# Performance work log

Hardware: AMD Instinct MI355X
Metric: run time of the kernel (lower is better)

## Reference

```python
import jax, jax.numpy as jnp
import numpy as np

B, C_IN, N, K = 4, 128, 2048, 16
DIM, POS, PH, AH = 256, 3, 64, 256 * 4
EPS = 1e-5


def _conv1x1(x, W, b):
    # 1x1 Conv2d: x (B, Cin, n, k) -> (B, Cout, n, k)
    return jnp.einsum('oc,bcnk->bonk', W, x) + b[None, :, None, None]


def _bn(x, gamma, beta, mean, var):
    # eval-mode BatchNorm2d with running stats
    scale = gamma / jnp.sqrt(var + EPS)
    return x * scale[None, :, None, None] + (beta - mean * scale)[None, :, None, None]


def _forward(key, values, pos, Wk, bk, Wq, bq, Wv, bv,
             Wp1, bp1, pg, pb, pm, pv, Wp2, bp2,
             Wa1, ba1, ag, ab, am, av, Wa2, ba2, We, be):
    b, _, n, k = key.shape
    pos_f = jnp.broadcast_to(pos[:, :, :, None], (b, pos.shape[1], n, k))
    kf = _conv1x1(key, Wk, bk)          # (B, dim, n, k)
    v = _conv1x1(values, Wv, bv)        # (B, dim, n, k)
    q = _conv1x1(pos_f, Wq, bq)         # (B, dim, n, k)
    qk_rel = q - kf
    pe = _conv1x1(jax.nn.relu(_bn(_conv1x1(q, Wp1, bp1), pg, pb, pm, pv)), Wp2, bp2)
    attn = _conv1x1(jax.nn.relu(_bn(_conv1x1(qk_rel * pe + pe, Wa1, ba1), ag, ab, am, av)), Wa2, ba2)
    attn = jax.nn.softmax(attn, axis=-1)  # softmax over k neighbors
    agg = jnp.einsum('bcnk,bcnk->bcn', attn, v + pe)  # (B, dim, n)
    return jnp.einsum('oc,bcn->bon', We, agg) + be[None, :, None]


def setup_inputs():
    ks = jax.random.split(jax.random.key(0), 12)
    s = 0.02
    f32 = jnp.float32
    return {
        'key': jax.random.normal(ks[0], (B, C_IN, N, K), f32),
        'values': jax.random.normal(ks[1], (B, C_IN, N, K), f32),
        'pos': jax.random.normal(ks[2], (B, POS, N), f32),
        'Wk': jax.random.normal(ks[3], (DIM, C_IN), f32) * s,
        'bk': jnp.zeros((DIM,), f32),
        'Wq': jax.random.normal(ks[4], (DIM, POS), f32) * s,
        'bq': jnp.zeros((DIM,), f32),
        'Wv': jax.random.normal(ks[5], (DIM, C_IN), f32) * s,
        'bv': jnp.zeros((DIM,), f32),
        'Wp1': jax.random.normal(ks[6], (PH, DIM), f32) * s,
        'bp1': jnp.zeros((PH,), f32),
        'pg': jnp.ones((PH,), f32),
        'pb': jnp.zeros((PH,), f32),
        'pm': jnp.zeros((PH,), f32),
        'pv': jnp.ones((PH,), f32),
        'Wp2': jax.random.normal(ks[7], (DIM, PH), f32) * s,
        'bp2': jnp.zeros((DIM,), f32),
        'Wa1': jax.random.normal(ks[8], (AH, DIM), f32) * s,
        'ba1': jnp.zeros((AH,), f32),
        'ag': jnp.ones((AH,), f32),
        'ab': jnp.zeros((AH,), f32),
        'am': jnp.zeros((AH,), f32),
        'av': jnp.ones((AH,), f32),
        'Wa2': jax.random.normal(ks[9], (DIM, AH), f32) * s,
        'ba2': jnp.zeros((DIM,), f32),
        'We': jax.random.normal(ks[10], (DIM, DIM), f32) * s,
        'be': jnp.zeros((DIM,), f32),
    }


def reference(key, values, pos, Wk, bk, Wq, bq, Wv, bv,
              Wp1, bp1, pg, pb, pm, pv, Wp2, bp2,
              Wa1, ba1, ag, ab, am, av, Wa2, ba2, We, be):
    return _forward(key, values, pos, Wk, bk, Wq, bq, Wv, bv,
                    Wp1, bp1, pg, pb, pm, pv, Wp2, bp2,
                    Wa1, ba1, ag, ab, am, av, Wa2, ba2, We, be)
```

## Files before the change

kernel.cpp:

```cpp
#include <hip/hip_runtime.h>
#include <math.h>

typedef __attribute__((ext_vector_type(8))) short bf16x8;
typedef __attribute__((ext_vector_type(4))) float f32x4;

namespace {
constexpr int NN   = 2048;
constexpr float EPSV = 1e-5f;

constexpr size_t WK_O   = 0;
constexpr size_t WV_O   = 65536;
constexpr size_t B1F_O  = 131072;
constexpr size_t WEP_O  = 135168;
constexpr size_t WA1I_O = 266240;
constexpr size_t WA2I_O = 790528;
constexpr size_t WP1Q_O = 1314816;
constexpr size_t SC_O   = 1315840;
constexpr size_t WS_TOTAL = 1319936;

constexpr int X_OFF   = 0;
constexpr int WC_OFF  = 65536;
constexpr int WA2C_OFF= 98304;
constexpr int HR_OFF  = 131072;
constexpr int PE_OFF  = 147456;
constexpr int H1_OFF  = 151552;
constexpr int POS_OFF = 153600;
constexpr int LDS_TOTAL = 153728;
}

__device__ __forceinline__ unsigned short f2bf(float x) {
    unsigned u = __float_as_uint(x);
    unsigned r = (u + 0x7FFFu + ((u >> 16) & 1u)) >> 16;
    return (unsigned short)r;
}
__device__ __forceinline__ float bf2f(unsigned short h) {
    return __uint_as_float(((unsigned)h) << 16);
}


__global__ void prep_sc(const float* __restrict__ ag,  const float* __restrict__ ab,
                        const float* __restrict__ am,  const float* __restrict__ av,
                        const float* __restrict__ ba1,
                        const float* __restrict__ Wp1, const float* __restrict__ Wq,
                        const float* __restrict__ bq,  const float* __restrict__ bp1,
                        const float* __restrict__ pg,  const float* __restrict__ pb,
                        const float* __restrict__ pm,  const float* __restrict__ pv,
                        char* __restrict__ ws)
{
    const int t = threadIdx.x, blk = blockIdx.x;
    float* b1f  = (float*)(ws + B1F_O);
    float* sc_s = (float*)(ws + SC_O);
    float* wp1q = (float*)(ws + WP1Q_O);
    if (blk < 4) {
        int j = blk * 256 + t;
        float sc = ag[j] * rsqrtf(av[j] + EPSV);
        sc_s[j] = sc;
        b1f[j] = ba1[j] * sc + ab[j] - am[j] * sc;
    } else if (t < 64) {
        int ph = t;
        float scp = pg[ph] * rsqrtf(pv[ph] + EPSV);
        float a0 = 0.f, a1 = 0.f, a2 = 0.f, abv = 0.f;
        for (int c = 0; c < 256; ++c) {
            float wv = Wp1[ph * 256 + c];
            a0 = fmaf(wv, Wq[c * 3 + 0], a0);
            a1 = fmaf(wv, Wq[c * 3 + 1], a1);
            a2 = fmaf(wv, Wq[c * 3 + 2], a2);
            abv = fmaf(wv, bq[c], abv);
        }
        wp1q[ph * 4 + 0] = scp * a0;
        wp1q[ph * 4 + 1] = scp * a1;
        wp1q[ph * 4 + 2] = scp * a2;
        wp1q[ph * 4 + 3] = scp * (abv + bp1[ph]) + (pb[ph] - pm[ph] * scp);
    }
}

__global__ void prep_cvt(const float* __restrict__ Wk, const float* __restrict__ Wv,
                         const float* __restrict__ We, const float* __restrict__ Wa1,
                         const float* __restrict__ Wa2, char* __restrict__ ws)
{
    const int idx = blockIdx.x * 256 + threadIdx.x;
    unsigned short* wk  = (unsigned short*)(ws + WK_O);
    unsigned short* wv  = (unsigned short*)(ws + WV_O);
    unsigned short* wep = (unsigned short*)(ws + WEP_O);
    unsigned short* w1i = (unsigned short*)(ws + WA1I_O);
    unsigned short* w2i = (unsigned short*)(ws + WA2I_O);
    const float* sc_s = (const float*)(ws + SC_O);
    if (idx < 32768) {
        wk[idx] = f2bf(Wk[idx]);
    } else if (idx < 65536) {
        int i = idx - 32768; wv[i] = f2bf(Wv[i]);
    } else if (idx < 131072) {
        int i = idx - 65536; wep[i] = f2bf(We[i]);
    } else if (idx < 393216) {
        int e = idx - 131072;
        int j = e >> 8, c = e & 255;
        float val = sc_s[j] * Wa1[e];
        int cc = j >> 6, jl = j & 63;
        int byte = cc * 32768 + (((jl << 9) + (c << 1)) ^ ((jl & 7) << 4));
        w1i[byte >> 1] = f2bf(val);
    } else {
        int e = idx - 393216;
        int o = e >> 10, j = e & 1023;
        int cc = j >> 6, jl = j & 63;
        int byte = cc * 32768 + (((o << 7) + (jl << 1)) ^ ((o & 7) << 4));
        w2i[byte >> 1] = f2bf(Wa2[e]);
    }
}

__global__ __launch_bounds__(256, 1)
void pt_main(const float* __restrict__ key, const float* __restrict__ values,
             const float* __restrict__ pos,
             const float* __restrict__ Wq,  const float* __restrict__ bq,
             const float* __restrict__ bk,  const float* __restrict__ bv,
             const float* __restrict__ Wp2, const float* __restrict__ bp2,
             const float* __restrict__ be,
             const char* __restrict__ ws,
             float* __restrict__ outp)
{
    extern __shared__ char sm[];
    const int t = threadIdx.x;
    const int w = t >> 6, l = t & 63;
    const int l15 = l & 15, lg = l >> 4;
    const int blk = blockIdx.x;
    const int b = blk >> 8;
    const int n0 = (blk & 255) * 8;
    const int wm0 = w * 32;

    const unsigned short* wkp = (const unsigned short*)(ws + WK_O);
    const unsigned short* wvp = (const unsigned short*)(ws + WV_O);
    const unsigned short* wep = (const unsigned short*)(ws + WEP_O);
    const float* b1f  = (const float*)(ws + B1F_O);
    const float* wp1q = (const float*)(ws + WP1Q_O);

    if (t < 24) {
        int nl = t / 3, p = t % 3;
        *(float*)(sm + POS_OFF + nl * 16 + p * 4) = pos[(b * 3 + p) * NN + n0 + nl];
    }
    {
        #pragma unroll
        for (int it = 0; it < 16; ++it) {
            int i = it * 256 + t;
            int clow = i & 7, k4 = (i >> 3) & 3, nl = (i >> 5) & 7, chigh = i >> 8;
            int c = chigh * 8 + clow;
            const float4 v = *(const float4*)(key + ((size_t)(b * 128 + c) * NN + (n0 + nl)) * 16 + k4 * 4);
            int m = nl * 16 + k4 * 4;
            #pragma unroll
            for (int j = 0; j < 4; ++j) {
                int mm = m + j;
                int byte = ((mm << 8) + (c << 1)) ^ ((mm & 7) << 4);
                float fj = (j == 0) ? v.x : (j == 1) ? v.y : (j == 2) ? v.z : v.w;
                *(unsigned short*)(sm + X_OFF + byte) = f2bf(fj);
            }
        }
    }
    __syncthreads();

    #pragma unroll
    for (int rep = 0; rep < 2; ++rep) {
        int idx = rep * 256 + t;
        int ph = idx >> 3, nl = idx & 7;
        const float4 wq4 = *(const float4*)(wp1q + ph * 4);
        float p0 = *(const float*)(sm + POS_OFF + nl * 16 + 0);
        float p1 = *(const float*)(sm + POS_OFF + nl * 16 + 4);
        float p2 = *(const float*)(sm + POS_OFF + nl * 16 + 8);
        float h = fmaf(wq4.x, p0, fmaf(wq4.y, p1, fmaf(wq4.z, p2, wq4.w)));
        *(float*)(sm + H1_OFF + ph * 32 + nl * 4) = fmaxf(h, 0.f);
    }
    __syncthreads();

    {
        float acc[8];
        #pragma unroll
        for (int n = 0; n < 8; ++n) acc[n] = 0.f;
        #pragma unroll 4
        for (int j = 0; j < 64; ++j) {
            float wv2 = Wp2[t * 64 + j];
            float4 ha = *(const float4*)(sm + H1_OFF + j * 32);
            float4 hb = *(const float4*)(sm + H1_OFF + j * 32 + 16);
            acc[0] = fmaf(wv2, ha.x, acc[0]); acc[1] = fmaf(wv2, ha.y, acc[1]);
            acc[2] = fmaf(wv2, ha.z, acc[2]); acc[3] = fmaf(wv2, ha.w, acc[3]);
            acc[4] = fmaf(wv2, hb.x, acc[4]); acc[5] = fmaf(wv2, hb.y, acc[5]);
            acc[6] = fmaf(wv2, hb.z, acc[6]); acc[7] = fmaf(wv2, hb.w, acc[7]);
        }
        float bp = bp2[t];
        #pragma unroll
        for (int n = 0; n < 8; ++n)
            *(unsigned short*)(sm + PE_OFF + n * 512 + t * 2) = f2bf(acc[n] + bp);
    }

    bf16x8 ak[2][4];
    #pragma unroll
    for (int mt = 0; mt < 2; ++mt)
        #pragma unroll
        for (int kt = 0; kt < 4; ++kt) {
            int m = wm0 + mt * 16 + l15, c = kt * 32 + lg * 8;
            ak[mt][kt] = *(const bf16x8*)(sm + X_OFF + (((m << 8) + (c << 1)) ^ ((m & 7) << 4)));
        }
    f32x4 zf = {0.f, 0.f, 0.f, 0.f};
    f32x4 kacc[2][16];
    #pragma unroll
    for (int mt = 0; mt < 2; ++mt)
        #pragma unroll
        for (int ot = 0; ot < 16; ++ot) kacc[mt][ot] = zf;
    #pragma unroll
    for (int ot = 0; ot < 16; ++ot) {
        #pragma unroll
        for (int kt = 0; kt < 4; ++kt) {
            int o = ot * 16 + l15, c = kt * 32 + lg * 8;
            bf16x8 bfr = *(const bf16x8*)(wkp + o * 128 + c);
            kacc[0][ot] = __builtin_amdgcn_mfma_f32_16x16x32_bf16(ak[0][kt], bfr, kacc[0][ot], 0, 0, 0);
            kacc[1][ot] = __builtin_amdgcn_mfma_f32_16x16x32_bf16(ak[1][kt], bfr, kacc[1][ot], 0, 0, 0);
        }
    }
    __syncthreads();

    #pragma unroll
    for (int mt = 0; mt < 2; ++mt) {
        const int nl = 2 * w + mt;
        float p0 = *(const float*)(sm + POS_OFF + nl * 16 + 0);
        float p1 = *(const float*)(sm + POS_OFF + nl * 16 + 4);
        float p2 = *(const float*)(sm + POS_OFF + nl * 16 + 8);
        #pragma unroll
        for (int ot = 0; ot < 16; ++ot) {
            int o = ot * 16 + l15;
            float q = fmaf(Wq[o * 3 + 0], p0, fmaf(Wq[o * 3 + 1], p1, fmaf(Wq[o * 3 + 2], p2, bq[o])));
            float pe = bf2f(*(const unsigned short*)(sm + PE_OFF + nl * 512 + o * 2));
            float bko = bk[o];
            #pragma unroll
            for (int r = 0; r < 4; ++r) {
                int m = wm0 + mt * 16 + lg * 4 + r;
                float x = (q - (kacc[mt][ot][r] + bko) + 1.f) * pe;
                *(unsigned short*)(sm + X_OFF + (((m << 9) + (o << 1)) ^ ((m & 7) << 4))) = f2bf(x);
            }
        }
    }

    f32x4 Y[2][16];
    #pragma unroll
    for (int mt = 0; mt < 2; ++mt)
        #pragma unroll
        for (int ot = 0; ot < 16; ++ot) Y[mt][ot] = zf;

    for (int cc = 0; cc < 16; ++cc) {
        if (cc) __syncthreads();
        {
            const float4* s1 = (const float4*)(ws + WA1I_O + (size_t)cc * 32768);
            float4* d1 = (float4*)(sm + WC_OFF);
            const float4* s2 = (const float4*)(ws + WA2I_O + (size_t)cc * 32768);
            float4* d2 = (float4*)(sm + WA2C_OFF);
            #pragma unroll
            for (int i = 0; i < 8; ++i) d1[i * 256 + t] = s1[i * 256 + t];
            #pragma unroll
            for (int i = 0; i < 8; ++i) d2[i * 256 + t] = s2[i * 256 + t];
        }
        __syncthreads();

        #pragma unroll
        for (int mt = 0; mt < 2; ++mt) {
            bf16x8 ax[8];
            #pragma unroll
            for (int kt = 0; kt < 8; ++kt) {
                int m = wm0 + mt * 16 + l15, c = kt * 32 + lg * 8;
                ax[kt] = *(const bf16x8*)(sm + X_OFF + (((m << 9) + (c << 1)) ^ ((m & 7) << 4)));
            }
            #pragma unroll
            for (int jt = 0; jt < 4; ++jt) {
                f32x4 acc = zf;
                #pragma unroll
                for (int kt = 0; kt < 8; ++kt) {
                    int jl = jt * 16 + l15, c2 = kt * 32 + lg * 8;
                    bf16x8 bw = *(const bf16x8*)(sm + WC_OFF + (((jl << 9) + (c2 << 1)) ^ ((jl & 7) << 4)));
                    acc = __builtin_amdgcn_mfma_f32_16x16x32_bf16(ax[kt], bw, acc, 0, 0, 0);
                }
                float b1v = b1f[cc * 64 + jt * 16 + l15];
                #pragma unroll
                for (int r = 0; r < 4; ++r) {
                    int ml = mt * 16 + lg * 4 + r, jl = jt * 16 + l15;
                    float hv = fmaxf(acc[r] + b1v, 0.f);
                    *(unsigned short*)(sm + HR_OFF + w * 4096 + (((ml << 7) + (jl << 1)) ^ ((ml & 7) << 4))) = f2bf(hv);
                }
            }
        }
        #pragma unroll
        for (int mt = 0; mt < 2; ++mt) {
            bf16x8 ah[2];
            #pragma unroll
            for (int kt = 0; kt < 2; ++kt) {
                int ml = mt * 16 + l15, jl = kt * 32 + lg * 8;
                ah[kt] = *(const bf16x8*)(sm + HR_OFF + w * 4096 + (((ml << 7) + (jl << 1)) ^ ((ml & 7) << 4)));
            }
            #pragma unroll
            for (int ot = 0; ot < 16; ++ot) {
                #pragma unroll
                for (int kt = 0; kt < 2; ++kt) {
                    int o = ot * 16 + l15, jl = kt * 32 + lg * 8;
                    bf16x8 bw = *(const bf16x8*)(sm + WA2C_OFF + (((o << 7) + (jl << 1)) ^ ((o & 7) << 4)));
                    Y[mt][ot] = __builtin_amdgcn_mfma_f32_16x16x32_bf16(ah[kt], bw, Y[mt][ot], 0, 0, 0);
                }
            }
        }
    }
    __syncthreads();

    {
        #pragma unroll
        for (int it = 0; it < 16; ++it) {
            int i = it * 256 + t;
            int clow = i & 7, k4 = (i >> 3) & 3, nl = (i >> 5) & 7, chigh = i >> 8;
            int c = chigh * 8 + clow;
            const float4 v = *(const float4*)(values + ((size_t)(b * 128 + c) * NN + (n0 + nl)) * 16 + k4 * 4);
            int m = nl * 16 + k4 * 4;
            #pragma unroll
            for (int j = 0; j < 4; ++j) {
                int mm = m + j;
                int byte = ((mm << 8) + (c << 1)) ^ ((mm & 7) << 4);
                float fj = (j == 0) ? v.x : (j == 1) ? v.y : (j == 2) ? v.z : v.w;
                *(unsigned short*)(sm + WC_OFF + byte) = f2bf(fj);
            }
        }
    }

    #pragma unroll
    for (int mt = 0; mt < 2; ++mt) {
        #pragma unroll
        for (int ot = 0; ot < 16; ++ot) {
            float mx = fmaxf(fmaxf(Y[mt][ot][0], Y[mt][ot][1]), fmaxf(Y[mt][ot][2], Y[mt][ot][3]));
            mx = fmaxf(mx, __shfl_xor(mx, 16));
            mx = fmaxf(mx, __shfl_xor(mx, 32));
            float e0 = expf(Y[mt][ot][0] - mx), e1 = expf(Y[mt][ot][1] - mx);
            float e2 = expf(Y[mt][ot][2] - mx), e3 = expf(Y[mt][ot][3] - mx);
            float s = e0 + e1 + e2 + e3;
            s += __shfl_xor(s, 16);
            s += __shfl_xor(s, 32);
            float inv = 1.f / s;
            Y[mt][ot][0] = e0 * inv; Y[mt][ot][1] = e1 * inv;
            Y[mt][ot][2] = e2 * inv; Y[mt][ot][3] = e3 * inv;
        }
    }
    __syncthreads();

    bf16x8 av_[2][4];
    #pragma unroll
    for (int mt = 0; mt < 2; ++mt)
        #pragma unroll
        for (int kt = 0; kt < 4; ++kt) {
            int m = wm0 + mt * 16 + l15, c = kt * 32 + lg * 8;
            av_[mt][kt] = *(const bf16x8*)(sm + WC_OFF + (((m << 8) + (c << 1)) ^ ((m & 7) << 4)));
        }
    #pragma unroll
    for (int ot = 0; ot < 16; ++ot) {
        int o = ot * 16 + l15;
        f32x4 vacc[2];
        vacc[0] = zf; vacc[1] = zf;
        #pragma unroll
        for (int kt = 0; kt < 4; ++kt) {
            int c = kt * 32 + lg * 8;
            bf16x8 bfr = *(const bf16x8*)(wvp + o * 128 + c);
            vacc[0] = __builtin_amdgcn_mfma_f32_16x16x32_bf16(av_[0][kt], bfr, vacc[0], 0, 0, 0);
            vacc[1] = __builtin_amdgcn_mfma_f32_16x16x32_bf16(av_[1][kt], bfr, vacc[1], 0, 0, 0);
        }
        float bvo = bv[o];
        #pragma unroll
        for (int mt = 0; mt < 2; ++mt) {
            int nl = 2 * w + mt;
            float s = 0.f;
            #pragma unroll
            for (int r = 0; r < 4; ++r)
                s = fmaf(Y[mt][ot][r], vacc[mt][r] + bvo, s);
            s += __shfl_xor(s, 16);
            s += __shfl_xor(s, 32);
            float agg = s + bf2f(*(const unsigned short*)(sm + PE_OFF + nl * 512 + o * 2));
            if (lg == 0)
                *(unsigned short*)(sm + X_OFF + (((nl << 9) + (o << 1)) ^ ((nl & 7) << 4))) = f2bf(agg);
        }
    }
    __syncthreads();

    bf16x8 aa[8];
    #pragma unroll
    for (int kt = 0; kt < 8; ++kt) {
        int row = l15, c = kt * 32 + lg * 8;
        aa[kt] = *(const bf16x8*)(sm + X_OFF + (((row << 9) + (c << 1)) ^ ((row & 7) << 4)));
    }
    #pragma unroll
    for (int ot = 0; ot < 4; ++ot) {
        int oo = w * 64 + ot * 16 + l15;
        f32x4 acc = zf;
        #pragma unroll
        for (int kt = 0; kt < 8; ++kt) {
            int c = kt * 32 + lg * 8;
            bf16x8 bfr = *(const bf16x8*)(wep + oo * 256 + c);
            acc = __builtin_amdgcn_mfma_f32_16x16x32_bf16(aa[kt], bfr, acc, 0, 0, 0);
        }
        if (lg < 2) {
            float bev = be[oo];
            float4 vv;
            vv.x = acc[0] + bev; vv.y = acc[1] + bev;
            vv.z = acc[2] + bev; vv.w = acc[3] + bev;
            *(float4*)(outp + ((size_t)(b * 256 + oo)) * NN + n0 + lg * 4) = vv;
        }
    }
}

extern "C" void kernel_launch(void* const* d_in, const int* in_sizes, int n_in,
                              void* d_out, int out_size, void* d_ws, size_t ws_size,
                              hipStream_t stream) {
    const float* key    = (const float*)d_in[0];
    const float* values = (const float*)d_in[1];
    const float* pos    = (const float*)d_in[2];
    const float* Wk     = (const float*)d_in[3];
    const float* bk     = (const float*)d_in[4];
    const float* Wq     = (const float*)d_in[5];
    const float* bq     = (const float*)d_in[6];
    const float* Wv     = (const float*)d_in[7];
    const float* bv     = (const float*)d_in[8];
    const float* Wp1    = (const float*)d_in[9];
    const float* bp1    = (const float*)d_in[10];
    const float* pg     = (const float*)d_in[11];
    const float* pb     = (const float*)d_in[12];
    const float* pm     = (const float*)d_in[13];
    const float* pv     = (const float*)d_in[14];
    const float* Wp2    = (const float*)d_in[15];
    const float* bp2    = (const float*)d_in[16];
    const float* Wa1    = (const float*)d_in[17];
    const float* ba1    = (const float*)d_in[18];
    const float* ag     = (const float*)d_in[19];
    const float* ab     = (const float*)d_in[20];
    const float* am     = (const float*)d_in[21];
    const float* av     = (const float*)d_in[22];
    const float* Wa2    = (const float*)d_in[23];
    const float* We     = (const float*)d_in[25];
    const float* be     = (const float*)d_in[26];
    (void)in_sizes; (void)n_in; (void)out_size; (void)ws_size;

    char* ws = (char*)d_ws;

    hipFuncSetAttribute((const void*)pt_main,
                        hipFuncAttributeMaxDynamicSharedMemorySize, LDS_TOTAL);

    hipLaunchKernelGGL(prep_sc, dim3(5), dim3(256), 0, stream,
                       ag, ab, am, av, ba1, Wp1, Wq, bq, bp1, pg, pb, pm, pv, ws);
    hipLaunchKernelGGL(prep_cvt, dim3(2560), dim3(256), 0, stream,
                       Wk, Wv, We, Wa1, Wa2, ws);
    hipLaunchKernelGGL(pt_main, dim3(1024), dim3(256), LDS_TOTAL, stream,
                       key, values, pos, Wq, bq, bk, bv, Wp2, bp2, be,
                       (const char*)ws, (float*)d_out);
}
```

Baseline: 480.8 us.

## Make main kernel warp-private with per-wave LDS and direct global weight reads

The main kernel is restructured so each wave owns its two points and a private LDS scratch area. The Wa1 and Wa2 weights are read straight from global/L2 instead of being staged cooperatively through LDS with block barriers. LDS shrinks from about 150KB to 72KB and launch bounds allow two blocks per CU. The Wp2 positional MLP moves to registers via shuffles, and the weight conversion kernel is vectorised to four elements per thread. The risks are more global-memory traffic for weights and register pressure from the held key loads and accumulators.

```diff
diff --git a/kernel.cpp b/kernel.cpp
--- a/kernel.cpp
+++ b/kernel.cpp
@@ -5,27 +5,21 @@
 typedef __attribute__((ext_vector_type(4))) float f32x4;
 
 namespace {
-constexpr int NN   = 2048;
+constexpr int NN = 2048;
 constexpr float EPSV = 1e-5f;
 
 constexpr size_t WK_O   = 0;
 constexpr size_t WV_O   = 65536;
 constexpr size_t B1F_O  = 131072;
 constexpr size_t WEP_O  = 135168;
-constexpr size_t WA1I_O = 266240;
-constexpr size_t WA2I_O = 790528;
+constexpr size_t W1I_O  = 266240;
+constexpr size_t W2I_O  = 790528;
 constexpr size_t WP1Q_O = 1314816;
 constexpr size_t SC_O   = 1315840;
-constexpr size_t WS_TOTAL = 1319936;
-
-constexpr int X_OFF   = 0;
-constexpr int WC_OFF  = 65536;
-constexpr int WA2C_OFF= 98304;
-constexpr int HR_OFF  = 131072;
-constexpr int PE_OFF  = 147456;
-constexpr int H1_OFF  = 151552;
-constexpr int POS_OFF = 153600;
-constexpr int LDS_TOTAL = 153728;
+
+constexpr int SCR_SZ   = 16384;
+constexpr int PE_OFF   = 65536;
+constexpr int LDS_TOTAL = 73728;
 }
 
 __device__ __forceinline__ unsigned short f2bf(float x) {
@@ -78,36 +72,26 @@
                          const float* __restrict__ We, const float* __restrict__ Wa1,
                          const float* __restrict__ Wa2, char* __restrict__ ws)
 {
-    const int idx = blockIdx.x * 256 + threadIdx.x;
-    unsigned short* wk  = (unsigned short*)(ws + WK_O);
-    unsigned short* wv  = (unsigned short*)(ws + WV_O);
-    unsigned short* wep = (unsigned short*)(ws + WEP_O);
-    unsigned short* w1i = (unsigned short*)(ws + WA1I_O);
-    unsigned short* w2i = (unsigned short*)(ws + WA2I_O);
+    const int idx4 = blockIdx.x * 256 + threadIdx.x;
+    if (idx4 >= 163840) return;
+    const int e0 = idx4 * 4;
     const float* sc_s = (const float*)(ws + SC_O);
-    if (idx < 32768) {
-        wk[idx] = f2bf(Wk[idx]);
-    } else if (idx < 65536) {
-        int i = idx - 32768; wv[i] = f2bf(Wv[i]);
-    } else if (idx < 131072) {
-        int i = idx - 65536; wep[i] = f2bf(We[i]);
-    } else if (idx < 393216) {
-        int e = idx - 131072;
-        int j = e >> 8, c = e & 255;
-        float val = sc_s[j] * Wa1[e];
-        int cc = j >> 6, jl = j & 63;
-        int byte = cc * 32768 + (((jl << 9) + (c << 1)) ^ ((jl & 7) << 4));
-        w1i[byte >> 1] = f2bf(val);
-    } else {
-        int e = idx - 393216;
-        int o = e >> 10, j = e & 1023;
-        int cc = j >> 6, jl = j & 63;
-        int byte = cc * 32768 + (((o << 7) + (jl << 1)) ^ ((o & 7) << 4));
-        w2i[byte >> 1] = f2bf(Wa2[e]);
-    }
-}
-
-__global__ __launch_bounds__(256, 1)
+    const float* src;
+    unsigned short* dst;
+    float scale = 1.f;
+    if (e0 < 32768)       { src = Wk + e0;            dst = (unsigned short*)(ws + WK_O)  + e0; }
+    else if (e0 < 65536)  { int e = e0 - 32768;  src = Wv  + e; dst = (unsigned short*)(ws + WV_O)  + e; }
+    else if (e0 < 131072) { int e = e0 - 65536;  src = We  + e; dst = (unsigned short*)(ws + WEP_O) + e; }
+    else if (e0 < 393216) { int e = e0 - 131072; src = Wa1 + e; dst = (unsigned short*)(ws + W1I_O) + e; scale = sc_s[e >> 8]; }
+    else                  { int e = e0 - 393216; src = Wa2 + e; dst = (unsigned short*)(ws + W2I_O) + e; }
+    float4 v = *(const float4*)src;
+    ushort4 o;
+    o.x = f2bf(v.x * scale); o.y = f2bf(v.y * scale);
+    o.z = f2bf(v.z * scale); o.w = f2bf(v.w * scale);
+    *(ushort4*)dst = o;
+}
+
+__global__ __launch_bounds__(256, 2)
 void pt_main(const float* __restrict__ key, const float* __restrict__ values,
              const float* __restrict__ pos,
              const float* __restrict__ Wq,  const float* __restrict__ bq,
@@ -124,199 +108,208 @@
     const int blk = blockIdx.x;
     const int b = blk >> 8;
     const int n0 = (blk & 255) * 8;
-    const int wm0 = w * 32;
+
+    char* scw = sm + w * SCR_SZ;
+    char* pew = sm + PE_OFF + w * 2048;
 
     const unsigned short* wkp = (const unsigned short*)(ws + WK_O);
     const unsigned short* wvp = (const unsigned short*)(ws + WV_O);
     const unsigned short* wep = (const unsigned short*)(ws + WEP_O);
+    const unsigned short* w1p = (const unsigned short*)(ws + W1I_O);
+    const unsigned short* w2p = (const unsigned short*)(ws + W2I_O);
     const float* b1f  = (const float*)(ws + B1F_O);
     const float* wp1q = (const float*)(ws + WP1Q_O);
 
-    if (t < 24) {
-        int nl = t / 3, p = t % 3;
-        *(float*)(sm + POS_OFF + nl * 16 + p * 4) = pos[(b * 3 + p) * NN + n0 + nl];
-    }
+    const f32x4 zf = {0.f, 0.f, 0.f, 0.f};
+
+    const int kq = l & 3, nv = (l >> 2) & 1, c8 = l >> 3;
+    float4 kreg[16];
     {
-        #pragma unroll
-        for (int it = 0; it < 16; ++it) {
-            int i = it * 256 + t;
-            int clow = i & 7, k4 = (i >> 3) & 3, nl = (i >> 5) & 7, chigh = i >> 8;
-            int c = chigh * 8 + clow;
-            const float4 v = *(const float4*)(key + ((size_t)(b * 128 + c) * NN + (n0 + nl)) * 16 + k4 * 4);
-            int m = nl * 16 + k4 * 4;
+        const float* kb = key + ((size_t)b * 128 * NN + (size_t)(n0 + 2 * w + nv)) * 16 + kq * 4;
+        #pragma unroll
+        for (int i = 0; i < 16; ++i) {
+            int c = i * 8 + c8;
+            kreg[i] = *(const float4*)(kb + (size_t)c * NN * 16);
+        }
+    }
+
+    float p_[2][3];
+    {
+        const float4 wq4 = *(const float4*)(wp1q + l * 4);
+        float h1v[2];
+        #pragma unroll
+        for (int nl = 0; nl < 2; ++nl) {
+            int n = n0 + 2 * w + nl;
+            p_[nl][0] = pos[(b * 3 + 0) * NN + n];
+            p_[nl][1] = pos[(b * 3 + 1) * NN + n];
+            p_[nl][2] = pos[(b * 3 + 2) * NN + n];
+            h1v[nl] = fmaxf(fmaf(wq4.x, p_[nl][0],
+                            fmaf(wq4.y, p_[nl][1],
+                            fmaf(wq4.z, p_[nl][2], wq4.w))), 0.f);
+        }
+        float pacc[2][4];
+        #pragma unroll
+        for (int nl = 0; nl < 2; ++nl)
+            #pragma unroll
+            for (int oi = 0; oi < 4; ++oi) pacc[nl][oi] = 0.f;
+        #pragma unroll 4
+        for (int j4 = 0; j4 < 16; ++j4) {
+            float h0[4], h1[4];
+            #pragma unroll
+            for (int jj = 0; jj < 4; ++jj) {
+                h0[jj] = __shfl(h1v[0], j4 * 4 + jj);
+                h1[jj] = __shfl(h1v[1], j4 * 4 + jj);
+            }
+            #pragma unroll
+            for (int oi = 0; oi < 4; ++oi) {
+                const float4 wv4 = *(const float4*)(Wp2 + (oi * 64 + l) * 64 + j4 * 4);
+                pacc[0][oi] = fmaf(wv4.x, h0[0], fmaf(wv4.y, h0[1], fmaf(wv4.z, h0[2], fmaf(wv4.w, h0[3], pacc[0][oi]))));
+                pacc[1][oi] = fmaf(wv4.x, h1[0], fmaf(wv4.y, h1[1], fmaf(wv4.z, h1[2], fmaf(wv4.w, h1[3], pacc[1][oi]))));
+            }
+        }
+        #pragma unroll
+        for (int oi = 0; oi < 4; ++oi) {
+            int o = oi * 64 + l;
+            float bp = bp2[o], bko = bk[o], bqo = bq[o];
+            float wq0 = Wq[o * 3 + 0], wq1 = Wq[o * 3 + 1], wq2 = Wq[o * 3 + 2];
+            #pragma unroll
+            for (int nl = 0; nl < 2; ++nl) {
+                float pe = pacc[nl][oi] + bp;
+                float q  = fmaf(wq0, p_[nl][0], fmaf(wq1, p_[nl][1], fmaf(wq2, p_[nl][2], bqo)));
+                *(unsigned short*)(pew + nl * 512 + o * 2)        = f2bf((q + 1.f - bko) * pe);
+                *(unsigned short*)(pew + 1024 + nl * 512 + o * 2) = f2bf(pe);
+            }
+        }
+    }
+
+    #pragma unroll
+    for (int i = 0; i < 16; ++i) {
+        int c = i * 8 + c8;
+        float4 v = kreg[i];
+        #pragma unroll
+        for (int j = 0; j < 4; ++j) {
+            int m = nv * 16 + kq * 4 + j;
+            float fj = (j == 0) ? v.x : (j == 1) ? v.y : (j == 2) ? v.z : v.w;
+            *(unsigned short*)(scw + ((m * 256 + c * 2) ^ ((m & 7) << 4))) = f2bf(fj);
+        }
+    }
+
+    bf16x8 kB[2][4];
+    #pragma unroll
+    for (int mt = 0; mt < 2; ++mt)
+        #pragma unroll
+        for (int kt = 0; kt < 4; ++kt) {
+            int ml = mt * 16 + l15;
+            kB[mt][kt] = *(const bf16x8*)(scw + ((ml * 256 + kt * 64 + lg * 16) ^ ((ml & 7) << 4)));
+        }
+    f32x4 kacc[2][16];
+    #pragma unroll
+    for (int mt = 0; mt < 2; ++mt)
+        #pragma unroll
+        for (int ot = 0; ot < 16; ++ot) kacc[mt][ot] = zf;
+    #pragma unroll 4
+    for (int ot = 0; ot < 16; ++ot) {
+        #pragma unroll
+        for (int kt = 0; kt < 4; ++kt) {
+            bf16x8 aW = *(const bf16x8*)(wkp + (ot * 16 + l15) * 128 + kt * 32 + lg * 8);
+            kacc[0][ot] = __builtin_amdgcn_mfma_f32_16x16x32_bf16(aW, kB[0][kt], kacc[0][ot], 0, 0, 0);
+            kacc[1][ot] = __builtin_amdgcn_mfma_f32_16x16x32_bf16(aW, kB[1][kt], kacc[1][ot], 0, 0, 0);
+        }
+    }
+
+    #pragma unroll
+    for (int mt = 0; mt < 2; ++mt) {
+        const int ml = mt * 16 + l15;
+        #pragma unroll
+        for (int ot = 0; ot < 16; ++ot) {
+            int o0 = ot * 16 + lg * 4;
+            ushort4 qv  = *(const ushort4*)(pew + mt * 512 + o0 * 2);
+            ushort4 pv4 = *(const ushort4*)(pew + 1024 + mt * 512 + o0 * 2);
+            ushort4 pk;
+            pk.x = f2bf(bf2f(qv.x) - kacc[mt][ot][0] * bf2f(pv4.x));
+            pk.y = f2bf(bf2f(qv.y) - kacc[mt][ot][1] * bf2f(pv4.y));
+            pk.z = f2bf(bf2f(qv.z) - kacc[mt][ot][2] * bf2f(pv4.z));
+            pk.w = f2bf(bf2f(qv.w) - kacc[mt][ot][3] * bf2f(pv4.w));
+            *(ushort4*)(scw + ((ml * 512 + o0 * 2) ^ ((ml & 7) << 4))) = pk;
+        }
+    }
+
+    bf16x8 ax[2][8];
+    #pragma unroll
+    for (int mt = 0; mt < 2; ++mt)
+        #pragma unroll
+        for (int kt = 0; kt < 8; ++kt) {
+            int ml = mt * 16 + l15;
+            ax[mt][kt] = *(const bf16x8*)(scw + ((ml * 512 + kt * 64 + lg * 16) ^ ((ml & 7) << 4)));
+        }
+
+    {
+        const float* vb = values + ((size_t)b * 128 * NN + (size_t)(n0 + 2 * w + nv)) * 16 + kq * 4;
+        float4 vreg[16];
+        #pragma unroll
+        for (int i = 0; i < 16; ++i) {
+            int c = i * 8 + c8;
+            vreg[i] = *(const float4*)(vb + (size_t)c * NN * 16);
+        }
+        #pragma unroll
+        for (int i = 0; i < 16; ++i) {
+            int c = i * 8 + c8;
+            float4 v = vreg[i];
             #pragma unroll
             for (int j = 0; j < 4; ++j) {
-                int mm = m + j;
-                int byte = ((mm << 8) + (c << 1)) ^ ((mm & 7) << 4);
+                int m = nv * 16 + kq * 4 + j;
                 float fj = (j == 0) ? v.x : (j == 1) ? v.y : (j == 2) ? v.z : v.w;
-                *(unsigned short*)(sm + X_OFF + byte) = f2bf(fj);
-            }
-        }
-    }
-    __syncthreads();
-
-    #pragma unroll
-    for (int rep = 0; rep < 2; ++rep) {
-        int idx = rep * 256 + t;
-        int ph = idx >> 3, nl = idx & 7;
-        const float4 wq4 = *(const float4*)(wp1q + ph * 4);
-        float p0 = *(const float*)(sm + POS_OFF + nl * 16 + 0);
-        float p1 = *(const float*)(sm + POS_OFF + nl * 16 + 4);
-        float p2 = *(const float*)(sm + POS_OFF + nl * 16 + 8);
-        float h = fmaf(wq4.x, p0, fmaf(wq4.y, p1, fmaf(wq4.z, p2, wq4.w)));
-        *(float*)(sm + H1_OFF + ph * 32 + nl * 4) = fmaxf(h, 0.f);
-    }
-    __syncthreads();
-
-    {
-        float acc[8];
-        #pragma unroll
-        for (int n = 0; n < 8; ++n) acc[n] = 0.f;
-        #pragma unroll 4
-        for (int j = 0; j < 64; ++j) {
-            float wv2 = Wp2[t * 64 + j];
-            float4 ha = *(const float4*)(sm + H1_OFF + j * 32);
-            float4 hb = *(const float4*)(sm + H1_OFF + j * 32 + 16);
-            acc[0] = fmaf(wv2, ha.x, acc[0]); acc[1] = fmaf(wv2, ha.y, acc[1]);
-            acc[2] = fmaf(wv2, ha.z, acc[2]); acc[3] = fmaf(wv2, ha.w, acc[3]);
-            acc[4] = fmaf(wv2, hb.x, acc[4]); acc[5] = fmaf(wv2, hb.y, acc[5]);
-            acc[6] = fmaf(wv2, hb.z, acc[6]); acc[7] = fmaf(wv2, hb.w, acc[7]);
-        }
-        float bp = bp2[t];
-        #pragma unroll
-        for (int n = 0; n < 8; ++n)
-            *(unsigned short*)(sm + PE_OFF + n * 512 + t * 2) = f2bf(acc[n] + bp);
-    }
-
-    bf16x8 ak[2][4];
+                *(unsigned short*)(scw + ((m * 256 + c * 2) ^ ((m & 7) << 4))) = f2bf(fj);
+            }
+        }
+    }
+
+    f32x4 Y[2][16];
     #pragma unroll
     for (int mt = 0; mt < 2; ++mt)
         #pragma unroll
-        for (int kt = 0; kt < 4; ++kt) {
-            int m = wm0 + mt * 16 + l15, c = kt * 32 + lg * 8;
-            ak[mt][kt] = *(const bf16x8*)(sm + X_OFF + (((m << 8) + (c << 1)) ^ ((m & 7) << 4)));
-        }
-    f32x4 zf = {0.f, 0.f, 0.f, 0.f};
-    f32x4 kacc[2][16];
-    #pragma unroll
-    for (int mt = 0; mt < 2; ++mt)
-        #pragma unroll
-        for (int ot = 0; ot < 16; ++ot) kacc[mt][ot] = zf;
-    #pragma unroll
-    for (int ot = 0; ot < 16; ++ot) {
-        #pragma unroll
-        for (int kt = 0; kt < 4; ++kt) {
-            int o = ot * 16 + l15, c = kt * 32 + lg * 8;
-            bf16x8 bfr = *(const bf16x8*)(wkp + o * 128 + c);
-            kacc[0][ot] = __builtin_amdgcn_mfma_f32_16x16x32_bf16(ak[0][kt], bfr, kacc[0][ot], 0, 0, 0);
-            kacc[1][ot] = __builtin_amdgcn_mfma_f32_16x16x32_bf16(ak[1][kt], bfr, kacc[1][ot], 0, 0, 0);
-        }
-    }
-    __syncthreads();
-
-    #pragma unroll
-    for (int mt = 0; mt < 2; ++mt) {
-        const int nl = 2 * w + mt;
-        float p0 = *(const float*)(sm + POS_OFF + nl * 16 + 0);
-        float p1 = *(const float*)(sm + POS_OFF + nl * 16 + 4);
-        float p2 = *(const float*)(sm + POS_OFF + nl * 16 + 8);
-        #pragma unroll
-        for (int ot = 0; ot < 16; ++ot) {
-            int o = ot * 16 + l15;
-            float q = fmaf(Wq[o * 3 + 0], p0, fmaf(Wq[o * 3 + 1], p1, fmaf(Wq[o * 3 + 2], p2, bq[o])));
-            float pe = bf2f(*(const unsigned short*)(sm + PE_OFF + nl * 512 + o * 2));
-            float bko = bk[o];
-            #pragma unroll
-            for (int r = 0; r < 4; ++r) {
-                int m = wm0 + mt * 16 + lg * 4 + r;
-                float x = (q - (kacc[mt][ot][r] + bko) + 1.f) * pe;
-                *(unsigned short*)(sm + X_OFF + (((m << 9) + (o << 1)) ^ ((m & 7) << 4))) = f2bf(x);
-            }
-        }
-    }
-
-    f32x4 Y[2][16];
-    #pragma unroll
-    for (int mt = 0; mt < 2; ++mt)
-        #pragma unroll
         for (int ot = 0; ot < 16; ++ot) Y[mt][ot] = zf;
 
-    for (int cc = 0; cc < 16; ++cc) {
-        if (cc) __syncthreads();
-        {
-            const float4* s1 = (const float4*)(ws + WA1I_O + (size_t)cc * 32768);
-            float4* d1 = (float4*)(sm + WC_OFF);
-            const float4* s2 = (const float4*)(ws + WA2I_O + (size_t)cc * 32768);
-            float4* d2 = (float4*)(sm + WA2C_OFF);
-            #pragma unroll
-            for (int i = 0; i < 8; ++i) d1[i * 256 + t] = s1[i * 256 + t];
-            #pragma unroll
-            for (int i = 0; i < 8; ++i) d2[i * 256 + t] = s2[i * 256 + t];
-        }
-        __syncthreads();
-
-        #pragma unroll
-        for (int mt = 0; mt < 2; ++mt) {
-            bf16x8 ax[8];
+    char* hrb = scw + 8192;
+    #pragma unroll 1
+    for (int cc = 0; cc < 32; ++cc) {
+        f32x4 a1[2][2];
+        a1[0][0] = zf; a1[0][1] = zf; a1[1][0] = zf; a1[1][1] = zf;
+        #pragma unroll
+        for (int jt = 0; jt < 2; ++jt) {
+            const unsigned short* wr = w1p + (size_t)(cc * 32 + jt * 16 + l15) * 256 + lg * 8;
             #pragma unroll
             for (int kt = 0; kt < 8; ++kt) {
-                int m = wm0 + mt * 16 + l15, c = kt * 32 + lg * 8;
-                ax[kt] = *(const bf16x8*)(sm + X_OFF + (((m << 9) + (c << 1)) ^ ((m & 7) << 4)));
-            }
-            #pragma unroll
-            for (int jt = 0; jt < 4; ++jt) {
-                f32x4 acc = zf;
-                #pragma unroll
-                for (int kt = 0; kt < 8; ++kt) {
-                    int jl = jt * 16 + l15, c2 = kt * 32 + lg * 8;
-                    bf16x8 bw = *(const bf16x8*)(sm + WC_OFF + (((jl << 9) + (c2 << 1)) ^ ((jl & 7) << 4)));
-                    acc = __builtin_amdgcn_mfma_f32_16x16x32_bf16(ax[kt], bw, acc, 0, 0, 0);
-                }
-                float b1v = b1f[cc * 64 + jt * 16 + l15];
+                bf16x8 bW = *(const bf16x8*)(wr + kt * 32);
+                a1[0][jt] = __builtin_amdgcn_mfma_f32_16x16x32_bf16(ax[0][kt], bW, a1[0][jt], 0, 0, 0);
+                a1[1][jt] = __builtin_amdgcn_mfma_f32_16x16x32_bf16(ax[1][kt], bW, a1[1][jt], 0, 0, 0);
+            }
+        }
+        #pragma unroll
+        for (int jt = 0; jt < 2; ++jt) {
+            float b1 = b1f[cc * 32 + jt * 16 + l15];
+            #pragma unroll
+            for (int mt = 0; mt < 2; ++mt) {
                 #pragma unroll
                 for (int r = 0; r < 4; ++r) {
-                    int ml = mt * 16 + lg * 4 + r, jl = jt * 16 + l15;
-                    float hv = fmaxf(acc[r] + b1v, 0.f);
-                    *(unsigned short*)(sm + HR_OFF + w * 4096 + (((ml << 7) + (jl << 1)) ^ ((ml & 7) << 4))) = f2bf(hv);
+                    int ml = mt * 16 + lg * 4 + r;
+                    int jl = jt * 16 + l15;
+                    float hv = fmaxf(a1[mt][jt][r] + b1, 0.f);
+                    *(unsigned short*)(hrb + ((ml * 64 + jl * 2) ^ (((ml >> 2) & 3) << 4))) = f2bf(hv);
                 }
             }
         }
+        bf16x8 ah[2];
         #pragma unroll
         for (int mt = 0; mt < 2; ++mt) {
-            bf16x8 ah[2];
-            #pragma unroll
-            for (int kt = 0; kt < 2; ++kt) {
-                int ml = mt * 16 + l15, jl = kt * 32 + lg * 8;
-                ah[kt] = *(const bf16x8*)(sm + HR_OFF + w * 4096 + (((ml << 7) + (jl << 1)) ^ ((ml & 7) << 4)));
-            }
-            #pragma unroll
-            for (int ot = 0; ot < 16; ++ot) {
-                #pragma unroll
-                for (int kt = 0; kt < 2; ++kt) {
-                    int o = ot * 16 + l15, jl = kt * 32 + lg * 8;
-                    bf16x8 bw = *(const bf16x8*)(sm + WA2C_OFF + (((o << 7) + (jl << 1)) ^ ((o & 7) << 4)));
-                    Y[mt][ot] = __builtin_amdgcn_mfma_f32_16x16x32_bf16(ah[kt], bw, Y[mt][ot], 0, 0, 0);
-                }
-            }
-        }
-    }
-    __syncthreads();
-
-    {
-        #pragma unroll
-        for (int it = 0; it < 16; ++it) {
-            int i = it * 256 + t;
-            int clow = i & 7, k4 = (i >> 3) & 3, nl = (i >> 5) & 7, chigh = i >> 8;
-            int c = chigh * 8 + clow;
-            const float4 v = *(const float4*)(values + ((size_t)(b * 128 + c) * NN + (n0 + nl)) * 16 + k4 * 4);
-            int m = nl * 16 + k4 * 4;
-            #pragma unroll
-            for (int j = 0; j < 4; ++j) {
-                int mm = m + j;
-                int byte = ((mm << 8) + (c << 1)) ^ ((mm & 7) << 4);
-                float fj = (j == 0) ? v.x : (j == 1) ? v.y : (j == 2) ? v.z : v.w;
-                *(unsigned short*)(sm + WC_OFF + byte) = f2bf(fj);
-            }
+            int ml = mt * 16 + l15;
+            ah[mt] = *(const bf16x8*)(hrb + ((ml * 64 + lg * 16) ^ (((ml >> 2) & 3) << 4)));
+        }
+        #pragma unroll
+        for (int ot = 0; ot < 16; ++ot) {
+            bf16x8 bW2 = *(const bf16x8*)(w2p + (size_t)(ot * 16 + l15) * 1024 + cc * 32 + lg * 8);
+            Y[0][ot] = __builtin_amdgcn_mfma_f32_16x16x32_bf16(ah[0], bW2, Y[0][ot], 0, 0, 0);
+            Y[1][ot] = __builtin_amdgcn_mfma_f32_16x16x32_bf16(ah[1], bW2, Y[1][ot], 0, 0, 0);
         }
     }
 
@@ -337,60 +330,66 @@
             Y[mt][ot][2] = e2 * inv; Y[mt][ot][3] = e3 * inv;
         }
     }
-    __syncthreads();
-
-    bf16x8 av_[2][4];
+
+    bf16x8 vB[2][4];
     #pragma unroll
     for (int mt = 0; mt < 2; ++mt)
         #pragma unroll
         for (int kt = 0; kt < 4; ++kt) {
-            int m = wm0 + mt * 16 + l15, c = kt * 32 + lg * 8;
-            av_[mt][kt] = *(const bf16x8*)(sm + WC_OFF + (((m << 8) + (c << 1)) ^ ((m & 7) << 4)));
-        }
-    #pragma unroll
+            int ml = mt * 16 + l15;
+            vB[mt][kt] = *(const bf16x8*)(scw + ((ml * 256 + kt * 64 + lg * 16) ^ ((ml & 7) << 4)));
+        }
+    float aggv[2][16];
+    #pragma unroll 4
     for (int ot = 0; ot < 16; ++ot) {
         int o = ot * 16 + l15;
-        f32x4 vacc[2];
-        vacc[0] = zf; vacc[1] = zf;
+        f32x4 v0 = zf, v1 = zf;
         #pragma unroll
         for (int kt = 0; kt < 4; ++kt) {
-            int c = kt * 32 + lg * 8;
-            bf16x8 bfr = *(const bf16x8*)(wvp + o * 128 + c);
-            vacc[0] = __builtin_amdgcn_mfma_f32_16x16x32_bf16(av_[0][kt], bfr, vacc[0], 0, 0, 0);
-            vacc[1] = __builtin_amdgcn_mfma_f32_16x16x32_bf16(av_[1][kt], bfr, vacc[1], 0, 0, 0);
+            bf16x8 bWv = *(const bf16x8*)(wvp + o * 128 + kt * 32 + lg * 8);
+            v0 = __builtin_amdgcn_mfma_f32_16x16x32_bf16(vB[0][kt], bWv, v0, 0, 0, 0);
+            v1 = __builtin_amdgcn_mfma_f32_16x16x32_bf16(vB[1][kt], bWv, v1, 0, 0, 0);
         }
         float bvo = bv[o];
+        #pragma unroll
+        for (int mt = 0; mt < 2; ++mt) {
+            f32x4 va = mt ? v1 : v0;
+            float s = Y[mt][ot][0] * (va[0] + bvo);
+            s = fmaf(Y[mt][ot][1], va[1] + bvo, s);
+            s = fmaf(Y[mt][ot][2], va[2] + bvo, s);
+            s = fmaf(Y[mt][ot][3], va[3] + bvo, s);
+            s += __shfl_xor(s, 16);
+            s += __shfl_xor(s, 32);
+            aggv[mt][ot] = s + bf2f(*(const unsigned short*)(pew + 1024 + mt * 512 + o * 2));
+        }
+    }
+
+    __syncthreads();
+    if (lg == 0) {
         #pragma unroll
         for (int mt = 0; mt < 2; ++mt) {
             int nl = 2 * w + mt;
-            float s = 0.f;
-            #pragma unroll
-            for (int r = 0; r < 4; ++r)
-                s = fmaf(Y[mt][ot][r], vacc[mt][r] + bvo, s);
-            s += __shfl_xor(s, 16);
-            s += __shfl_xor(s, 32);
-            float agg = s + bf2f(*(const unsigned short*)(sm + PE_OFF + nl * 512 + o * 2));
-            if (lg == 0)
-                *(unsigned short*)(sm + X_OFF + (((nl << 9) + (o << 1)) ^ ((nl & 7) << 4))) = f2bf(agg);
+            #pragma unroll
+            for (int ot = 0; ot < 16; ++ot) {
+                int o = ot * 16 + l15;
+                *(unsigned short*)(sm + PE_OFF + ((nl * 512 + o * 2) ^ ((nl & 7) << 4))) = f2bf(aggv[mt][ot]);
+            }
         }
     }
     __syncthreads();
 
     bf16x8 aa[8];
     #pragma unroll
-    for (int kt = 0; kt < 8; ++kt) {
-        int row = l15, c = kt * 32 + lg * 8;
-        aa[kt] = *(const bf16x8*)(sm + X_OFF + (((row << 9) + (c << 1)) ^ ((row & 7) << 4)));
-    }
+    for (int kt = 0; kt < 8; ++kt)
+        aa[kt] = *(const bf16x8*)(sm + PE_OFF + ((l15 * 512 + kt * 64 + lg * 16) ^ ((l15 & 7) << 4)));
     #pragma unroll
     for (int ot = 0; ot < 4; ++ot) {
         int oo = w * 64 + ot * 16 + l15;
         f32x4 acc = zf;
         #pragma unroll
         for (int kt = 0; kt < 8; ++kt) {
-            int c = kt * 32 + lg * 8;
-            bf16x8 bfr = *(const bf16x8*)(wep + oo * 256 + c);
-            acc = __builtin_amdgcn_mfma_f32_16x16x32_bf16(aa[kt], bfr, acc, 0, 0, 0);
+            bf16x8 bWe = *(const bf16x8*)(wep + oo * 256 + kt * 32 + lg * 8);
+            acc = __builtin_amdgcn_mfma_f32_16x16x32_bf16(aa[kt], bWe, acc, 0, 0, 0);
         }
         if (lg < 2) {
             float bev = be[oo];
@@ -440,7 +439,7 @@
 
     hipLaunchKernelGGL(prep_sc, dim3(5), dim3(256), 0, stream,
                        ag, ab, am, av, ba1, Wp1, Wq, bq, bp1, pg, pb, pm, pv, ws);
-    hipLaunchKernelGGL(prep_cvt, dim3(2560), dim3(256), 0, stream,
+    hipLaunchKernelGGL(prep_cvt, dim3(640), dim3(256), 0, stream,
                        Wk, Wv, We, Wa1, Wa2, ws);
     hipLaunchKernelGGL(pt_main, dim3(1024), dim3(256), LDS_TOTAL, stream,
                        key, values, pos, Wq, bq, bk, bv, Wp2, bp2, be,
```

Result: slower. 775.1 us (+61.2%).
